# Optimization experiments

Measured on AMD Instinct MI355X. Metric: run time of the kernel, lower is better.

## Reference

```python
import jax, jax.numpy as jnp
import numpy as np
from math import comb

F = 32           # features
NB = 8           # num_basis_functions
N_ITER = 3       # num_iterations
CUTOFF = 5.0
MAXZ = 17        # max_atomic_number
NDCM = 4
N_NODES = 10000
N_EDGES = 160000
OFF = (0, 1, 4)  # start index of degree l block in the (L+1)^2=9 axis
WID = (1, 3, 5)
DEG = np.array([0, 1, 1, 1, 2, 2, 2, 2, 2])


def _sph_harm(u):
    # Real spherical harmonics up to l=2, Racah normalization, cartesian order.
    x, y, z = u[..., 0], u[..., 1], u[..., 2]
    s3 = 3.0 ** 0.5
    return jnp.stack([
        jnp.ones_like(x),
        x, y, z,
        s3 * x * y, s3 * y * z, 0.5 * (3.0 * z * z - 1.0), s3 * x * z,
        0.5 * s3 * (x * x - y * y),
    ], axis=-1)


def _gaunt():
    # Exact Gaunt (triple-product) coupling coefficients via spherical quadrature:
    # Gauss-Legendre (8 pts) in cos(theta) x 16 uniform pts in phi is exact for
    # products of three degree<=2 harmonics. Odd-parity (l1+l2+l3 odd) entries
    # integrate to zero, which matches include_pseudotensors=False.
    t, w = np.polynomial.legendre.leggauss(8)
    phi = np.arange(16) * (2.0 * np.pi / 16.0)
    st = np.sqrt(1.0 - t * t)
    pts = np.stack([
        st[:, None] * np.cos(phi)[None, :],
        st[:, None] * np.sin(phi)[None, :],
        t[:, None] * np.ones_like(phi)[None, :],
    ], axis=-1).reshape(-1, 3)
    wts = np.repeat(w / 32.0, 16)  # mean over sphere
    Y = np.asarray(_sph_harm(jnp.asarray(pts)))
    G = np.einsum('k,kp,kq,kr->pqr', wts, Y, Y, Y)
    G[np.abs(G) < 1e-10] = 0.0
    return G.astype(np.float32)


GAUNT = _gaunt()  # (9, 9, 9)
MP_PATHS = [(a, b, c) for a in range(3) for b in range(3) for c in range(3)
            if (a + b + c) % 2 == 0 and abs(a - b) <= c <= a + b]
TD_PATHS = [p for p in MP_PATHS if p[2] <= 1]


def _blk(l):
    return slice(OFF[l], OFF[l] + WID[l])


def _edge_basis(positions, dst_idx, src_idx):
    d = positions[src_idx] - positions[dst_idx]          # (E, 3)
    r2 = jnp.sum(d * d, axis=-1)
    r = jnp.sqrt(jnp.maximum(r2, 1e-12))
    Y = _sph_harm(d / r[:, None])                        # (E, 9)
    rc = jnp.minimum(r, CUTOFF - 1e-6)                   # safe smooth_cutoff
    cut = jnp.where(r < CUTOFF,
                    jnp.exp(-(rc * rc) / ((CUTOFF - rc) * (CUTOFF + rc))), 0.0)
    yv = 1.0 / (1.0 + r)                                 # reciprocal mapping
    k = jnp.arange(NB)
    binom = jnp.asarray([float(comb(NB - 1, i)) for i in range(NB)], dtype=jnp.float32)
    rbf = binom * yv[:, None] ** k * (1.0 - yv[:, None]) ** (NB - 1 - k)
    return Y, rbf * cut[:, None]                         # (E,9), (E,NB)


def _message_pass(x, Y, rbf, dst_idx, src_idx, W, num_nodes):
    # msg[e,lm3,f] = sum G[lm1,lm2,lm3] x_src[e,lm1,f] Y[e,lm2] (rbf[e] @ W[l1,l2,l3])[f]
    xs = x[src_idx]                                      # (E, 9, F)
    parts = {0: [], 1: [], 2: []}
    for (l1, l2, l3) in MP_PATHS:
        rw = rbf @ W[l1, l2, l3]                         # (E, F) radial weights
        t = xs[:, _blk(l1), :] * rw[:, None, :]
        c = jnp.einsum('pqr,epf,eq->erf',
                       GAUNT[_blk(l1), _blk(l2), _blk(l3)], t, Y[:, _blk(l2)])
        parts[l3].append(c)
    msg = jnp.concatenate([sum(parts[l]) for l in range(3)], axis=1)
    return jax.ops.segment_sum(msg, dst_idx, num_segments=num_nodes)


def _dense(x, W, b):
    out = jnp.einsum('npf,pfg->npg', x, W[DEG])
    return out.at[:, 0, :].add(b)


def _silu_e3(x):
    # Gated equivariant silu: act(s) on scalars, x_lm * act'(s) for l>0.
    s = x[:, 0:1, :]
    sg = jax.nn.sigmoid(s)
    return jnp.concatenate([s * sg, x[:, 1:, :] * (sg * (1.0 + s * (1.0 - sg)))], axis=1)


def _tensor_dense(x, W):
    # with per-path feature-mixing weights; output (N, 4, NDCM).
    parts = {0: [], 1: []}
    for (l1, l2, l3) in TD_PATHS:
        c = jnp.einsum('pqr,npf,nqf,fg->nrg',
                       GAUNT[_blk(l1), _blk(l2), _blk(l3)],
                       x[:, _blk(l1), :], x[:, _blk(l2), :], W[l1, l2, l3])
        parts[l3].append(c)
    return jnp.concatenate([sum(parts[0]), sum(parts[1])], axis=1)


def _forward(positions, embed_table, mp_W, d1_W, d1_b, d2_W, d2_b, td_W,
             mono_W, element_bias, atomic_numbers, dst_idx, src_idx):
    n = positions.shape[0]
    Y, rbf = _edge_basis(positions, dst_idx, src_idx)
    x = jnp.zeros((n, 9, F), positions.dtype).at[:, 0, :].set(embed_table[atomic_numbers])
    for i in range(N_ITER):
        y = x + _message_pass(x, Y, rbf, dst_idx, src_idx, mp_W[i], n)
        y = _silu_e3(_dense(y, d1_W[i], d1_b[i]))
        y = _dense(y, d2_W[i], d2_b[i])
        x = x + y
    x2 = _tensor_dense(x, td_W)                          # (n, 4, NDCM)
    atomic_mono = x2[:, 0, :] @ mono_W + element_bias[atomic_numbers][:, None]
    # gated hard_tanh then * 0.3; dipole = l=1 components
    s = x2[:, 0:1, :]
    gate = ((s > -1.0) & (s < 1.0)).astype(x2.dtype)
    xh = jnp.concatenate([jnp.clip(s, -1.0, 1.0), x2[:, 1:, :] * gate], axis=1) * 0.3
    atomic_dipo = xh[:, 1:4, :]                          # (n, 3, NDCM)
    return atomic_mono, atomic_dipo


def setup_inputs() -> dict:
    key = jax.random.key(0)
    ks = jax.random.split(key, 12)
    atomic_numbers = jax.random.randint(ks[0], (N_NODES,), 0, MAXZ + 1)
    positions = jax.random.normal(ks[1], (N_NODES, 3), jnp.float32)
    dst_idx = jax.random.randint(ks[2], (N_EDGES,), 0, N_NODES)
    src_idx = jax.random.randint(ks[3], (N_EDGES,), 0, N_NODES)
    src_idx = jnp.where(src_idx == dst_idx, (src_idx + 1) % N_NODES, src_idx)
    embed_table = jax.random.normal(ks[4], (MAXZ + 1, F), jnp.float32)
    mp_W = jax.random.normal(ks[5], (N_ITER, 3, 3, 3, NB, F), jnp.float32) * 0.05
    d1_W = jax.random.normal(ks[6], (N_ITER, 3, F, F), jnp.float32) * (1.0 / F ** 0.5)
    d1_b = jnp.zeros((N_ITER, F), jnp.float32)
    d2_W = jax.random.normal(ks[7], (N_ITER, 3, F, F), jnp.float32) * (1.0 / F ** 0.5)
    d2_b = jnp.zeros((N_ITER, F), jnp.float32)
    td_W = jax.random.normal(ks[8], (3, 3, 2, F, NDCM), jnp.float32) * (1.0 / F)
    mono_W = jax.random.normal(ks[9], (NDCM, NDCM), jnp.float32) * (1.0 / NDCM ** 0.5)
    element_bias = jnp.zeros((MAXZ + 1,), jnp.float32)
    return {'positions': positions, 'embed_table': embed_table, 'mp_W': mp_W,
            'd1_W': d1_W, 'd1_b': d1_b, 'd2_W': d2_W, 'd2_b': d2_b,
            'td_W': td_W, 'mono_W': mono_W, 'element_bias': element_bias,
            'atomic_numbers': atomic_numbers, 'dst_idx': dst_idx, 'src_idx': src_idx}


def reference(positions, embed_table, mp_W, d1_W, d1_b, d2_W, d2_b, td_W,
              mono_W, element_bias, atomic_numbers, dst_idx, src_idx):
    return _forward(positions, embed_table, mp_W, d1_W, d1_b, d2_W, d2_b, td_W,
                    mono_W, element_bias, atomic_numbers, dst_idx, src_idx)
```

## Files before the change

kernel.cpp:

```cpp
#include <hip/hip_runtime.h>
#include <math.h>

#define NN 10000
#define NE 160000
#define MEPB 16
#define MT 256
#define CEPB 16

typedef float float2v __attribute__((ext_vector_type(2)));

namespace {
constexpr int kL1[11] = {0,0,0,1,1,1,1,2,2,2,2};
constexpr int kL2[11] = {0,1,2,0,1,1,2,0,1,2,2};
constexpr int kL3[11] = {0,1,2,1,0,2,1,2,1,0,2};
constexpr int kWOFF[11] = {0,5,7,10,12,14,16,20,22,24,26};
constexpr int tL1[7] = {0,0,1,1,1,2,2};
constexpr int tL2[7] = {0,1,0,1,2,1,2};
constexpr int tL3[7] = {0,1,1,0,1,1,0};
constexpr int kOFF[3] = {0,1,4};
constexpr int kWID[3] = {1,3,5};

struct TVT { unsigned char t[35], p[35]; };
constexpr TVT makeTV() {
  TVT v{};
  int ti = 0;
  for (int t = 0; t < 11; ++t)
    for (int i = 0; i < kWID[kL1[t]]; ++i) {
      v.t[ti] = (unsigned char)t;
      v.p[ti] = (unsigned char)(kOFF[kL1[t]] + i);
      ++ti;
    }
  return v;
}
constexpr TVT TV = makeTV();

struct CTb { unsigned char r[116], tv[116]; };
constexpr CTb makeCT() {
  CTb v{};
  int c = 0, ti = 0;
  for (int t = 0; t < 11; ++t)
    for (int i = 0; i < kWID[kL1[t]]; ++i) {
      for (int k = 0; k < kWID[kL3[t]]; ++k) {
        v.r[c]  = (unsigned char)(kOFF[kL3[t]] + k);
        v.tv[c] = (unsigned char)ti;
        ++c;
      }
      ++ti;
    }
  v.r[115] = 0; v.tv[115] = 0;
  return v;
}
constexpr CTb CTC = makeCT();
}

__device__ float GAUNT_d[729];
__device__ unsigned char CT_P_d[115], CT_R_d[115], CT_L2_d[115];

__device__ __forceinline__ float sphf(int c, float x, float y, float z) {
  const float s3 = 1.7320508075688772f;
  switch (c) {
    case 0: return 1.0f;
    case 1: return x;
    case 2: return y;
    case 3: return z;
    case 4: return s3 * x * y;
    case 5: return s3 * y * z;
    case 6: return 0.5f * (3.0f * z * z - 1.0f);
    case 7: return s3 * x * z;
    default: return 0.5f * s3 * (x * x - y * y);
  }
}

__global__ void gaunt_kernel() {
  __shared__ float Ysh[128][9];
  __shared__ double cph[16], sph[16];
  __shared__ double stq[8], tsh[8], wsh[8];
  const int idx = threadIdx.x;
  const double T[8] = {-0.9602898564975363, -0.7966664774136267, -0.5255324099163290, -0.1834346424956498,
                        0.1834346424956498,  0.5255324099163290,  0.7966664774136267,  0.9602898564975363};
  const double Wq[8] = {0.1012285362903763, 0.2223810344533745, 0.3137066458778873, 0.3626837833783620,
                        0.3626837833783620, 0.3137066458778873, 0.2223810344533745, 0.1012285362903763};
  if (idx < 16) {
    double phi = (double)idx * (6.283185307179586 / 16.0);
    cph[idx] = cos(phi);
    sph[idx] = sin(phi);
  }
  if (idx < 8) {
    tsh[idx] = T[idx];
    wsh[idx] = Wq[idx] / 32.0;
    stq[idx] = sqrt(1.0 - T[idx] * T[idx]);
  }
  __syncthreads();
  for (int i = idx; i < 128 * 9; i += 768) {
    int k = i / 9, c = i - k * 9;
    int it = k >> 4, ip = k & 15;
    float xf = (float)(stq[it] * cph[ip]);
    float yf = (float)(stq[it] * sph[ip]);
    float zf = (float)tsh[it];
    Ysh[k][c] = sphf(c, xf, yf, zf);
  }
  __syncthreads();
  if (idx < 729) {
    int p = idx / 81, q = (idx / 9) % 9, r = idx % 9;
    double acc = 0.0;
    for (int k = 0; k < 128; ++k)
      acc += wsh[k >> 4] * (double)Ysh[k][p] * (double)Ysh[k][q] * (double)Ysh[k][r];
    GAUNT_d[idx] = (fabs(acc) < 1e-10) ? 0.0f : (float)acc;
  }
  if (idx == 0) {
    int c = 0;
    for (int t = 0; t < 11; ++t) {
      int l1 = kL1[t], l2 = kL2[t], l3 = kL3[t];
      for (int i = 0; i < kWID[l1]; ++i)
        for (int k = 0; k < kWID[l3]; ++k) {
          CT_P_d[c]  = (unsigned char)(kOFF[l1] + i);
          CT_R_d[c]  = (unsigned char)(kOFF[l3] + k);
          CT_L2_d[c] = (unsigned char)l2;
          ++c;
        }
    }
  }
}

__global__ void hist_kernel(const int* __restrict__ dstI, int* __restrict__ cnt) {
  int e = blockIdx.x * 256 + threadIdx.x;
  if (e < NE) atomicAdd(&cnt[dstI[e]], 1);
}

__global__ void scan_kernel(int* __restrict__ wofs) {
  __shared__ int partial[1024];
  const int tid = threadIdx.x;
  const int base = tid * 10;
  int local[10];
  int s = 0;
  #pragma unroll
  for (int i = 0; i < 10; ++i) {
    int idx = base + i;
    int v = (idx < NN) ? wofs[idx] : 0;
    local[i] = s;
    s += v;
  }
  partial[tid] = s;
  __syncthreads();
  for (int off = 1; off < 1024; off <<= 1) {
    int v = (tid >= off) ? partial[tid - off] : 0;
    __syncthreads();
    partial[tid] += v;
    __syncthreads();
  }
  int pre = (tid == 0) ? 0 : partial[tid - 1];
  #pragma unroll
  for (int i = 0; i < 10; ++i) {
    int idx = base + i;
    if (idx < NN) wofs[idx] = pre + local[i];
  }
}

__global__ void edge_kernel(const float* __restrict__ pos,
                            const int* __restrict__ srcI, const int* __restrict__ dstI,
                            int* __restrict__ wofs, int* __restrict__ ssrc, int* __restrict__ sdst,
                            float* __restrict__ Yb, float* __restrict__ Rb) {
  int e = blockIdx.x * 256 + threadIdx.x;
  if (e >= NE) return;
  int s = srcI[e], d = dstI[e];
  float dx = pos[s * 3 + 0] - pos[d * 3 + 0];
  float dy = pos[s * 3 + 1] - pos[d * 3 + 1];
  float dz = pos[s * 3 + 2] - pos[d * 3 + 2];
  float r2 = dx * dx + dy * dy + dz * dz;
  float r = sqrtf(fmaxf(r2, 1e-12f));
  float inv = 1.0f / r;
  float x = dx * inv, y = dy * inv, z = dz * inv;
  const float s3 = 1.7320508075688772f;
  int sp = atomicAdd(&wofs[d], 1);
  ssrc[sp] = s;
  sdst[sp] = d;
  Yb[sp * 9 + 0] = 1.0f;
  Yb[sp * 9 + 1] = x;
  Yb[sp * 9 + 2] = y;
  Yb[sp * 9 + 3] = z;
  Yb[sp * 9 + 4] = s3 * x * y;
  Yb[sp * 9 + 5] = s3 * y * z;
  Yb[sp * 9 + 6] = 0.5f * (3.0f * z * z - 1.0f);
  Yb[sp * 9 + 7] = s3 * x * z;
  Yb[sp * 9 + 8] = 0.5f * s3 * (x * x - y * y);
  float rc = fminf(r, 5.0f - 1e-6f);
  float cut = (r < 5.0f) ? expf(-(rc * rc) / ((5.0f - rc) * (5.0f + rc))) : 0.0f;
  float yv = 1.0f / (1.0f + r);
  float om = 1.0f - yv;
  const float binom[8] = {1.f, 7.f, 21.f, 35.f, 35.f, 21.f, 7.f, 1.f};
  float yk[8], ok[8];
  yk[0] = 1.0f; ok[0] = 1.0f;
  #pragma unroll
  for (int k = 1; k < 8; ++k) { yk[k] = yk[k - 1] * yv; ok[k] = ok[k - 1] * om; }
  #pragma unroll
  for (int k = 0; k < 8; ++k) Rb[sp * 8 + k] = binom[k] * yk[k] * ok[7 - k] * cut;
}

__global__ void coef_kernel(const float* __restrict__ Yb, float* __restrict__ Cb) {
  __shared__ float Gs[729];
  __shared__ float Ys[CEPB][9];
  __shared__ unsigned char Tp[115], Tr[115], Tl2[115];
  const int tid = threadIdx.x;
  const int e0 = blockIdx.x * CEPB;
  for (int i = tid; i < 729; i += 256) Gs[i] = GAUNT_d[i];
  for (int i = tid; i < 115; i += 256) { Tp[i] = CT_P_d[i]; Tr[i] = CT_R_d[i]; Tl2[i] = CT_L2_d[i]; }
  for (int i = tid; i < CEPB * 9; i += 256) Ys[i / 9][i % 9] = Yb[e0 * 9 + i];
  __syncthreads();
  for (int i = tid; i < CEPB * 128; i += 256) {
    int ce = i >> 7, c = i & 127;
    if (c < 116) {
      float a = 0.0f;
      if (c < 115) {
        int p = Tp[c], r = Tr[c], l2 = Tl2[c];
        int q0 = (l2 == 0) ? 0 : ((l2 == 1) ? 1 : 4);
        int nq = (l2 == 0) ? 1 : ((l2 == 1) ? 3 : 5);
        for (int j = 0; j < nq; ++j) a += Gs[(p * 9 + q0 + j) * 9 + r] * Ys[ce][q0 + j];
      }
      Cb[(size_t)(e0 + ce) * 116 + c] = a;
    }
  }
}

__global__ void init_kernel(const float* __restrict__ embed, const int* __restrict__ Z,
                            float* __restrict__ xb, float* __restrict__ yb) {
  int idx = blockIdx.x * 256 + threadIdx.x;
  if (idx >= NN * 288) return;
  int n = idx / 288;
  int rem = idx - n * 288;
  int p = rem >> 5, f = rem & 31;
  xb[idx] = (p == 0) ? embed[Z[n] * 32 + f] : 0.0f;
  yb[idx] = 0.0f;
}

__launch_bounds__(MT, 8)
__global__ void message_kernel(const float* __restrict__ xb, float* __restrict__ yb,
                               const float* __restrict__ Rb, const float* __restrict__ Cb,
                               const float* __restrict__ Wg,
                               const int* __restrict__ ssrc, const int* __restrict__ sdst) {
  __shared__ __align__(16) float U[11 * 256];
  __shared__ __align__(16) float Cs[MEPB][116];
  __shared__ __align__(16) float Rs[MEPB][8];
  __shared__ int Ds[MEPB];
  __shared__ int Hs[2][9];
  __shared__ int nsegS[2];
  const int tid = threadIdx.x;
  const int e0 = blockIdx.x * MEPB;
  const int le = tid >> 4;
  const int f  = (tid & 15) * 2;

  const int sn = ssrc[e0 + le];
  float2v xs2[9];
  #pragma unroll
  for (int p = 0; p < 9; ++p) xs2[p] = *(const float2v*)&xb[sn * 288 + p * 32 + f];

  float* Ws = U;
  #pragma unroll
  for (int t = 0; t < 11; ++t) {
    const int off = kWOFF[t] * 256;
    Ws[t * 256 + tid] = Wg[off + tid];
  }
  {
    const float4* Cbv = (const float4*)Cb;
    float4* Csv = (float4*)Cs;
    #pragma unroll
    for (int i = tid; i < MEPB * 29; i += MT) Csv[i] = Cbv[(size_t)e0 * 29 + i];
  }
  for (int i = tid; i < MEPB * 8; i += MT) Rs[i >> 3][i & 7] = Rb[e0 * 8 + i];
  if (tid < MEPB) Ds[tid] = sdst[e0 + tid];
  __syncthreads();

  if (tid == 0) {
    #pragma unroll
    for (int b = 0; b < 2; ++b) {
      int ns = 0;
      #pragma unroll
      for (int i = 0; i < 8; ++i) {
        int gi = b * 8 + i;
        if (i == 0 || Ds[gi] != Ds[gi - 1]) Hs[b][ns++] = i;
      }
      Hs[b][ns] = 8;
      nsegS[b] = ns;
    }
  }

  float2v msg[9] = {{0.f,0.f},{0.f,0.f},{0.f,0.f},{0.f,0.f},{0.f,0.f},{0.f,0.f},{0.f,0.f},{0.f,0.f},{0.f,0.f}};
  int c = 0;
  #pragma unroll
  for (int t = 0; t < 11; ++t) {
    const float* base = &Ws[t * 256];
    float2v acc = {0.f, 0.f};
    #pragma unroll
    for (int k = 0; k < 8; ++k) {
      const float rv = Rs[le][k];
      const float2v rvv = {rv, rv};
      const float2v w2 = *(const float2v*)&base[k * 32 + f];
      acc = acc + rvv * w2;
    }
    const int o1 = kOFF[kL1[t]], w1 = kWID[kL1[t]];
    const int o3 = kOFF[kL3[t]], w3 = kWID[kL3[t]];
    #pragma unroll
    for (int i = 0; i < w1; ++i) {
      const float2v tvv = acc * xs2[o1 + i];
      #pragma unroll
      for (int k2 = 0; k2 < w3; ++k2) {
        const float cc = Cs[le][c]; ++c;
        const float2v ccv = {cc, cc};
        msg[o3 + k2] = msg[o3 + k2] + ccv * tvv;
      }
    }
  }

  float* Ms = U;
  #pragma unroll
  for (int b = 0; b < 2; ++b) {
    __syncthreads();
    if ((le >> 3) == b) {
      #pragma unroll
      for (int rr = 0; rr < 9; ++rr)
        *(float2v*)&Ms[(le & 7) * 288 + rr * 32 + f] = msg[rr];
    }
    __syncthreads();
    const int ns = nsegS[b];
    for (int i = tid; i < ns * 288; i += MT) {
      int s = i / 288, rf = i - s * 288;
      int h = Hs[b][s], hend = Hs[b][s + 1];
      float a = 0.0f;
      for (int e = h; e < hend; ++e) a += Ms[e * 288 + rf];
      atomicAdd(&yb[Ds[b * 8 + h] * 288 + rf], a);
    }
  }
}

__launch_bounds__(256)
__global__ void message_kernel_ic(const float* __restrict__ xb, float* __restrict__ yb,
                                  const float* __restrict__ Yb, const float* __restrict__ Rb,
                                  const float* __restrict__ Wg,
                                  const int* __restrict__ ssrc, const int* __restrict__ sdst) {
  __shared__ float Gs[729];
  __shared__ float Ws[11 * 256];
  __shared__ float Ys[8][9];
  __shared__ float Rs[8][8];
  __shared__ float Cs[8][116];
  __shared__ float Ms[8][288];
  __shared__ int Ds[8];
  __shared__ int Hs[9];
  __shared__ int nseg_s;
  __shared__ unsigned char Tp[115], Tr[115], Tl2[115];
  const int tid = threadIdx.x;
  const int e0 = blockIdx.x * 8;

  for (int i = tid; i < 729; i += 256) Gs[i] = GAUNT_d[i];
  for (int i = tid; i < 115; i += 256) { Tp[i] = CT_P_d[i]; Tr[i] = CT_R_d[i]; Tl2[i] = CT_L2_d[i]; }
  #pragma unroll
  for (int t = 0; t < 11; ++t) Ws[t * 256 + tid] = Wg[kWOFF[t] * 256 + tid];
  for (int i = tid; i < 8 * 16; i += 256) {
    int le = i >> 4, q = i & 15;
    if (q < 9) Ys[le][q] = Yb[(e0 + le) * 9 + q];
  }
  for (int i = tid; i < 8 * 8; i += 256) Rs[i >> 3][i & 7] = Rb[e0 * 8 + i];
  if (tid < 8) Ds[tid] = sdst[e0 + tid];
  __syncthreads();

  const int le = tid >> 5, f = tid & 31;
  const int sn = ssrc[e0 + le];
  float xs[9];
  #pragma unroll
  for (int p = 0; p < 9; ++p) xs[p] = xb[sn * 288 + p * 32 + f];

  for (int i = tid; i < 8 * 128; i += 256) {
    int ce = i >> 7, c = i & 127;
    if (c < 115) {
      int p = Tp[c], r = Tr[c], l2 = Tl2[c];
      int q0 = (l2 == 0) ? 0 : ((l2 == 1) ? 1 : 4);
      int nq = (l2 == 0) ? 1 : ((l2 == 1) ? 3 : 5);
      float a = 0.0f;
      for (int j = 0; j < nq; ++j) a += Gs[(p * 9 + q0 + j) * 9 + r] * Ys[ce][q0 + j];
      Cs[ce][c] = a;
    }
  }
  if (tid == 0) {
    int ns = 0;
    #pragma unroll
    for (int i = 0; i < 8; ++i)
      if (i == 0 || Ds[i] != Ds[i - 1]) Hs[ns++] = i;
    Hs[ns] = 8;
    nseg_s = ns;
  }
  __syncthreads();

  const float4 R0 = *(const float4*)&Rs[le][0];
  const float4 R1 = *(const float4*)&Rs[le][4];
  float rw[11];
  #pragma unroll
  for (int t = 0; t < 11; ++t) {
    const float* base = &Ws[t * 256];
    rw[t] = R0.x * base[f] + R0.y * base[32 + f] + R0.z * base[64 + f] + R0.w * base[96 + f]
          + R1.x * base[128 + f] + R1.y * base[160 + f] + R1.z * base[192 + f] + R1.w * base[224 + f];
  }
  float tv[35];
  #pragma unroll
  for (int j = 0; j < 35; ++j) tv[j] = rw[TV.t[j]] * xs[TV.p[j]];
  float msg[9] = {0.f, 0.f, 0.f, 0.f, 0.f, 0.f, 0.f, 0.f, 0.f};
  #pragma unroll
  for (int c = 0; c < 115; ++c) msg[CTC.r[c]] += Cs[le][c] * tv[CTC.tv[c]];
  #pragma unroll
  for (int rr = 0; rr < 9; ++rr) Ms[le][rr * 32 + f] = msg[rr];
  __syncthreads();

  const int nseg = nseg_s;
  for (int i = tid; i < nseg * 288; i += 256) {
    int s = i / 288, rf = i - s * 288;
    int h = Hs[s], hend = Hs[s + 1];
    float a = 0.0f;
    for (int e = h; e < hend; ++e) a += Ms[e][rf];
    atomicAdd(&yb[Ds[h] * 288 + rf], a);
  }
}

__global__ void dense_kernel(float* __restrict__ ybuf, float* __restrict__ xb,
                             const float* __restrict__ W1, const float* __restrict__ b1,
                             const float* __restrict__ W2, const float* __restrict__ b2) {
  __shared__ float yn[288];
  __shared__ float act[288];
  __shared__ float sb[32];
  const int n = blockIdx.x;
  const int tid = threadIdx.x;
  const int p = tid >> 5, g = tid & 31;
  const float xv = xb[n * 288 + tid];
  const float yv = ybuf[n * 288 + tid];
  ybuf[n * 288 + tid] = 0.0f;
  yn[tid] = xv + yv;
  __syncthreads();
  const int dg = (p == 0) ? 0 : ((p < 4) ? 1 : 2);
  float a = (p == 0) ? b1[g] : 0.0f;
  #pragma unroll
  for (int f = 0; f < 32; ++f) a += yn[p * 32 + f] * W1[(dg * 32 + f) * 32 + g];
  if (p == 0) sb[g] = a;
  __syncthreads();
  float s = sb[g];
  float sg = 1.0f / (1.0f + expf(-s));
  float v = (p == 0) ? s * sg : a * (sg * (1.0f + s * (1.0f - sg)));
  act[tid] = v;
  __syncthreads();
  float o = (p == 0) ? b2[g] : 0.0f;
  #pragma unroll
  for (int f = 0; f < 32; ++f) o += act[p * 32 + f] * W2[(dg * 32 + f) * 32 + g];
  xb[n * 288 + tid] = xv + o;
}

__global__ void dense_final_kernel(const float* __restrict__ ybuf, const float* __restrict__ xb,
                                   const float* __restrict__ W1, const float* __restrict__ b1,
                                   const float* __restrict__ W2, const float* __restrict__ b2,
                                   const float* __restrict__ tdW, const float* __restrict__ monoW,
                                   const float* __restrict__ ebias, const int* __restrict__ Z,
                                   float* __restrict__ out) {
  __shared__ float yn[288];
  __shared__ float act[288];
  __shared__ float sb[32];
  __shared__ float B[4][32];
  __shared__ float cb[16];
  const int n = blockIdx.x;
  const int tid = threadIdx.x;
  const int p = tid >> 5, g = tid & 31;
  const float xv = xb[n * 288 + tid];
  const float yv = ybuf[n * 288 + tid];
  yn[tid] = xv + yv;
  __syncthreads();
  const int dg = (p == 0) ? 0 : ((p < 4) ? 1 : 2);
  float a = (p == 0) ? b1[g] : 0.0f;
  #pragma unroll
  for (int f = 0; f < 32; ++f) a += yn[p * 32 + f] * W1[(dg * 32 + f) * 32 + g];
  if (p == 0) sb[g] = a;
  __syncthreads();
  float s = sb[g];
  float sg = 1.0f / (1.0f + expf(-s));
  float v = (p == 0) ? s * sg : a * (sg * (1.0f + s * (1.0f - sg)));
  act[tid] = v;
  __syncthreads();
  float o = (p == 0) ? b2[g] : 0.0f;
  #pragma unroll
  for (int f = 0; f < 32; ++f) o += act[p * 32 + f] * W2[(dg * 32 + f) * 32 + g];
  const float xnew = xv + o;
  __syncthreads();
  yn[tid] = xnew;
  __syncthreads();

  float creg = 0.0f;
  #pragma unroll
  for (int t = 0; t < 7; ++t) {
    const int l1 = tL1[t], l2 = tL2[t], l3 = tL3[t];
    const bool active = (tid < 128) && ((l3 == 0) ? (p == 0) : (p >= 1));
    float b = 0.0f;
    if (active) {
      #pragma unroll
      for (int i = 0; i < kWID[l1]; ++i) {
        const int pp = kOFF[l1] + i;
        float xp = yn[pp * 32 + g];
        #pragma unroll
        for (int j = 0; j < kWID[l2]; ++j) {
          const int q = kOFF[l2] + j;
          b += GAUNT_d[(pp * 9 + q) * 9 + p] * xp * yn[q * 32 + g];
        }
      }
    }
    if (tid < 128) B[p][g] = b;
    __syncthreads();
    if (active && g < 4) {
      const float* w = tdW + ((l1 * 3 + l2) * 2 + l3) * 128;
      float acc = 0.0f;
      #pragma unroll
      for (int f2 = 0; f2 < 32; ++f2) acc += B[p][f2] * w[f2 * 4 + g];
      creg += acc;
    }
    __syncthreads();
  }
  if (tid < 128 && g < 4) cb[p * 4 + g] = creg;
  __syncthreads();
  if (tid < 4) {
    int gg = tid;
    float m = 0.0f;
    #pragma unroll
    for (int j = 0; j < 4; ++j) m += cb[j] * monoW[j * 4 + gg];
    out[n * 4 + gg] = m + ebias[Z[n]];
  }
  if (tid < 12) {
    int row = tid / 4 + 1, gg = tid % 4;
    float sv = cb[gg];
    float gate = (sv > -1.0f && sv < 1.0f) ? 1.0f : 0.0f;
    out[NN * 4 + n * 12 + (row - 1) * 4 + gg] = cb[row * 4 + gg] * gate * 0.3f;
  }
}

extern "C" void kernel_launch(void* const* d_in, const int* in_sizes, int n_in,
                              void* d_out, int out_size, void* d_ws, size_t ws_size,
                              hipStream_t stream) {
  const float* positions = (const float*)d_in[0];
  const float* embed     = (const float*)d_in[1];
  const float* mpW       = (const float*)d_in[2];
  const float* d1W       = (const float*)d_in[3];
  const float* d1b       = (const float*)d_in[4];
  const float* d2W       = (const float*)d_in[5];
  const float* d2b       = (const float*)d_in[6];
  const float* tdW       = (const float*)d_in[7];
  const float* monoW     = (const float*)d_in[8];
  const float* ebias     = (const float*)d_in[9];
  const int* Z   = (const int*)d_in[10];
  const int* dst = (const int*)d_in[11];
  const int* src = (const int*)d_in[12];
  float* out = (float*)d_out;

  float* Yb = (float*)d_ws;
  float* Rb = Yb + (size_t)NE * 9;
  float* xb = Rb + (size_t)NE * 8;
  float* yb = xb + (size_t)NN * 288;
  size_t base_f = (size_t)NE * 9 + (size_t)NE * 8 + (size_t)NN * 288 * 2;
  size_t need_pc = (base_f + (size_t)NE * 116) * 4 + ((size_t)NE * 2 + NN) * 4;
  bool pc = ws_size >= need_pc;

  float* Cb = yb + (size_t)NN * 288;
  float* after = pc ? (Cb + (size_t)NE * 116) : Cb;
  int* ssrc = (int*)after;
  int* sdst = ssrc + NE;
  int* wofs = sdst + NE;

  gaunt_kernel<<<1, 768, 0, stream>>>();
  hipMemsetAsync(wofs, 0, NN * sizeof(int), stream);
  hist_kernel<<<NE / 256, 256, 0, stream>>>(dst, wofs);
  scan_kernel<<<1, 1024, 0, stream>>>(wofs);
  edge_kernel<<<NE / 256, 256, 0, stream>>>(positions, src, dst, wofs, ssrc, sdst, Yb, Rb);
  if (pc) coef_kernel<<<NE / CEPB, 256, 0, stream>>>(Yb, Cb);
  init_kernel<<<(NN * 288 + 255) / 256, 256, 0, stream>>>(embed, Z, xb, yb);

  for (int it = 0; it < 3; ++it) {
    if (pc)
      message_kernel<<<NE / MEPB, MT, 0, stream>>>(xb, yb, Rb, Cb, mpW + (size_t)it * 27 * 256, ssrc, sdst);
    else
      message_kernel_ic<<<NE / 8, 256, 0, stream>>>(xb, yb, Yb, Rb, mpW + (size_t)it * 27 * 256, ssrc, sdst);
    if (it < 2)
      dense_kernel<<<NN, 288, 0, stream>>>(yb, xb, d1W + (size_t)it * 3 * 1024, d1b + it * 32,
                                           d2W + (size_t)it * 3 * 1024, d2b + it * 32);
    else
      dense_final_kernel<<<NN, 288, 0, stream>>>(yb, xb, d1W + (size_t)it * 3 * 1024, d1b + it * 32,
                                                 d2W + (size_t)it * 3 * 1024, d2b + it * 32,
                                                 tdW, monoW, ebias, Z, out);
  }
}
```

Measured before the change: 433.8 us.

## Batch dense kernel over 8 nodes with shared-memory weights, split final readout

The dense update now handles 8 nodes per block, staging both weight matrices in shared memory once per block and prefetching the next node's inputs while the current one is computed. This is meant to cut repeated global weight reads and per-node block launch overhead. The final readout moves into a separate 128-thread kernel that runs after the last dense pass, which adds one launch and an extra read of the node features. Fewer blocks (1250) and 24KB of shared memory per block may reduce occupancy and parallelism.

```diff
diff --git a/kernel.cpp b/kernel.cpp
--- a/kernel.cpp
+++ b/kernel.cpp
@@ -6,6 +6,7 @@
 #define MEPB 16
 #define MT 256
 #define CEPB 16
+#define DNB 8
 
 typedef float float2v __attribute__((ext_vector_type(2)));
 
@@ -417,117 +418,106 @@
   }
 }
 
+__launch_bounds__(288)
 __global__ void dense_kernel(float* __restrict__ ybuf, float* __restrict__ xb,
                              const float* __restrict__ W1, const float* __restrict__ b1,
                              const float* __restrict__ W2, const float* __restrict__ b2) {
   __shared__ float yn[288];
   __shared__ float act[288];
   __shared__ float sb[32];
-  const int n = blockIdx.x;
+  __shared__ float W1s[3072];
+  __shared__ float W2s[3072];
   const int tid = threadIdx.x;
   const int p = tid >> 5, g = tid & 31;
-  const float xv = xb[n * 288 + tid];
-  const float yv = ybuf[n * 288 + tid];
-  ybuf[n * 288 + tid] = 0.0f;
-  yn[tid] = xv + yv;
-  __syncthreads();
   const int dg = (p == 0) ? 0 : ((p < 4) ? 1 : 2);
-  float a = (p == 0) ? b1[g] : 0.0f;
-  #pragma unroll
-  for (int f = 0; f < 32; ++f) a += yn[p * 32 + f] * W1[(dg * 32 + f) * 32 + g];
-  if (p == 0) sb[g] = a;
-  __syncthreads();
-  float s = sb[g];
-  float sg = 1.0f / (1.0f + expf(-s));
-  float v = (p == 0) ? s * sg : a * (sg * (1.0f + s * (1.0f - sg)));
-  act[tid] = v;
-  __syncthreads();
-  float o = (p == 0) ? b2[g] : 0.0f;
-  #pragma unroll
-  for (int f = 0; f < 32; ++f) o += act[p * 32 + f] * W2[(dg * 32 + f) * 32 + g];
-  xb[n * 288 + tid] = xv + o;
-}
-
-__global__ void dense_final_kernel(const float* __restrict__ ybuf, const float* __restrict__ xb,
-                                   const float* __restrict__ W1, const float* __restrict__ b1,
-                                   const float* __restrict__ W2, const float* __restrict__ b2,
-                                   const float* __restrict__ tdW, const float* __restrict__ monoW,
-                                   const float* __restrict__ ebias, const int* __restrict__ Z,
-                                   float* __restrict__ out) {
-  __shared__ float yn[288];
-  __shared__ float act[288];
-  __shared__ float sb[32];
+  for (int i = tid; i < 3072; i += 288) { W1s[i] = W1[i]; W2s[i] = W2[i]; }
+  const float b1v = b1[g], b2v = b2[g];
+  const int n0 = blockIdx.x * DNB;
+  float xv = xb[n0 * 288 + tid];
+  float yv = ybuf[n0 * 288 + tid];
+  __syncthreads();
+  for (int n = n0; n < n0 + DNB; ++n) {
+    yn[tid] = xv + yv;
+    ybuf[n * 288 + tid] = 0.0f;
+    __syncthreads();
+    float xv2 = 0.0f, yv2 = 0.0f;
+    if (n + 1 < n0 + DNB) {
+      xv2 = xb[(n + 1) * 288 + tid];
+      yv2 = ybuf[(n + 1) * 288 + tid];
+    }
+    float a = (p == 0) ? b1v : 0.0f;
+    #pragma unroll
+    for (int f = 0; f < 32; ++f) a += yn[p * 32 + f] * W1s[(dg * 32 + f) * 32 + g];
+    if (p == 0) sb[g] = a;
+    __syncthreads();
+    float s = sb[g];
+    float sg = 1.0f / (1.0f + expf(-s));
+    float v = (p == 0) ? s * sg : a * (sg * (1.0f + s * (1.0f - sg)));
+    act[tid] = v;
+    __syncthreads();
+    float o = (p == 0) ? b2v : 0.0f;
+    #pragma unroll
+    for (int f = 0; f < 32; ++f) o += act[p * 32 + f] * W2s[(dg * 32 + f) * 32 + g];
+    xb[n * 288 + tid] = xv + o;
+    __syncthreads();
+    xv = xv2; yv = yv2;
+  }
+}
+
+__global__ void final_kernel(const float* __restrict__ xb, const float* __restrict__ tdW,
+                             const float* __restrict__ monoW, const float* __restrict__ ebias,
+                             const int* __restrict__ Z, float* __restrict__ out) {
+  __shared__ float xl[288];
   __shared__ float B[4][32];
   __shared__ float cb[16];
   const int n = blockIdx.x;
   const int tid = threadIdx.x;
-  const int p = tid >> 5, g = tid & 31;
-  const float xv = xb[n * 288 + tid];
-  const float yv = ybuf[n * 288 + tid];
-  yn[tid] = xv + yv;
-  __syncthreads();
-  const int dg = (p == 0) ? 0 : ((p < 4) ? 1 : 2);
-  float a = (p == 0) ? b1[g] : 0.0f;
-  #pragma unroll
-  for (int f = 0; f < 32; ++f) a += yn[p * 32 + f] * W1[(dg * 32 + f) * 32 + g];
-  if (p == 0) sb[g] = a;
-  __syncthreads();
-  float s = sb[g];
-  float sg = 1.0f / (1.0f + expf(-s));
-  float v = (p == 0) ? s * sg : a * (sg * (1.0f + s * (1.0f - sg)));
-  act[tid] = v;
-  __syncthreads();
-  float o = (p == 0) ? b2[g] : 0.0f;
-  #pragma unroll
-  for (int f = 0; f < 32; ++f) o += act[p * 32 + f] * W2[(dg * 32 + f) * 32 + g];
-  const float xnew = xv + o;
-  __syncthreads();
-  yn[tid] = xnew;
-  __syncthreads();
-
+  const int r = tid >> 5, f = tid & 31;
+  for (int i = tid; i < 288; i += 128) xl[i] = xb[n * 288 + i];
+  __syncthreads();
   float creg = 0.0f;
   #pragma unroll
   for (int t = 0; t < 7; ++t) {
     const int l1 = tL1[t], l2 = tL2[t], l3 = tL3[t];
-    const bool active = (tid < 128) && ((l3 == 0) ? (p == 0) : (p >= 1));
+    const bool active = (l3 == 0) ? (r == 0) : (r >= 1);
     float b = 0.0f;
     if (active) {
       #pragma unroll
       for (int i = 0; i < kWID[l1]; ++i) {
-        const int pp = kOFF[l1] + i;
-        float xp = yn[pp * 32 + g];
+        const int p = kOFF[l1] + i;
+        float xp = xl[p * 32 + f];
         #pragma unroll
         for (int j = 0; j < kWID[l2]; ++j) {
           const int q = kOFF[l2] + j;
-          b += GAUNT_d[(pp * 9 + q) * 9 + p] * xp * yn[q * 32 + g];
+          b += GAUNT_d[(p * 9 + q) * 9 + r] * xp * xl[q * 32 + f];
         }
       }
     }
-    if (tid < 128) B[p][g] = b;
-    __syncthreads();
-    if (active && g < 4) {
+    B[r][f] = b;
+    __syncthreads();
+    if (f < 4 && active) {
       const float* w = tdW + ((l1 * 3 + l2) * 2 + l3) * 128;
       float acc = 0.0f;
       #pragma unroll
-      for (int f2 = 0; f2 < 32; ++f2) acc += B[p][f2] * w[f2 * 4 + g];
+      for (int f2 = 0; f2 < 32; ++f2) acc += B[r][f2] * w[f2 * 4 + f];
       creg += acc;
     }
     __syncthreads();
   }
-  if (tid < 128 && g < 4) cb[p * 4 + g] = creg;
+  if (f < 4) cb[r * 4 + f] = creg;
   __syncthreads();
   if (tid < 4) {
-    int gg = tid;
+    int g = tid;
     float m = 0.0f;
     #pragma unroll
-    for (int j = 0; j < 4; ++j) m += cb[j] * monoW[j * 4 + gg];
-    out[n * 4 + gg] = m + ebias[Z[n]];
+    for (int j = 0; j < 4; ++j) m += cb[j] * monoW[j * 4 + g];
+    out[n * 4 + g] = m + ebias[Z[n]];
   }
   if (tid < 12) {
-    int row = tid / 4 + 1, gg = tid % 4;
-    float sv = cb[gg];
-    float gate = (sv > -1.0f && sv < 1.0f) ? 1.0f : 0.0f;
-    out[NN * 4 + n * 12 + (row - 1) * 4 + gg] = cb[row * 4 + gg] * gate * 0.3f;
+    int row = tid / 4 + 1, g = tid % 4;
+    float s = cb[g];
+    float gate = (s > -1.0f && s < 1.0f) ? 1.0f : 0.0f;
+    out[NN * 4 + n * 12 + (row - 1) * 4 + g] = cb[row * 4 + g] * gate * 0.3f;
   }
 }
 
@@ -576,12 +566,8 @@
       message_kernel<<<NE / MEPB, MT, 0, stream>>>(xb, yb, Rb, Cb, mpW + (size_t)it * 27 * 256, ssrc, sdst);
     else
       message_kernel_ic<<<NE / 8, 256, 0, stream>>>(xb, yb, Yb, Rb, mpW + (size_t)it * 27 * 256, ssrc, sdst);
-    if (it < 2)
-      dense_kernel<<<NN, 288, 0, stream>>>(yb, xb, d1W + (size_t)it * 3 * 1024, d1b + it * 32,
-                                           d2W + (size_t)it * 3 * 1024, d2b + it * 32);
-    else
-      dense_final_kernel<<<NN, 288, 0, stream>>>(yb, xb, d1W + (size_t)it * 3 * 1024, d1b + it * 32,
-                                                 d2W + (size_t)it * 3 * 1024, d2b + it * 32,
-                                                 tdW, monoW, ebias, Z, out);
-  }
-}
+    dense_kernel<<<NN / DNB, 288, 0, stream>>>(yb, xb, d1W + (size_t)it * 3 * 1024, d1b + it * 32,
+                                               d2W + (size_t)it * 3 * 1024, d2b + it * 32);
+  }
+  final_kernel<<<NN, 128, 0, stream>>>(xb, tdW, monoW, ebias, Z, out);
+}
```

New measurement: 394.9 us. 1.1x faster.
